# Kernel optimization log

Hardware: AMD Instinct MI355X
Metric: run time of the kernel (lower is better)

Reference implementation:

```python
import jax, jax.numpy as jnp
import numpy as np

IGNORE_LABEL = -100  # config.data.ignore_label


def setup_inputs() -> dict:
    key = jax.random.key(0)
    k1, k2 = jax.random.split(key)
    V, D = 100000, 128            # voxel_num, feature dim of s_3d_output.F
    B, NV, H, W = 2, 4, 240, 320  # batch, n_views, height, width
    features_3d = jax.random.normal(k1, (V, D), dtype=jnp.float32)
    # raycast kernel output: per-pixel voxel index, or ignore_label for misses.
    raw = jax.random.randint(k2, (B, NV, H, W), 0, V + V // 4)
    indexes_image = jnp.where(raw < V, raw, IGNORE_LABEL).astype(jnp.int32)
    return {"features_3d": features_3d, "indexes_image": indexes_image}


def reference(features_3d, indexes_image):
    V = features_3d.shape[0]
    idx = indexes_image.reshape(-1)              # [P] flattened pixel->voxel index
    valid = idx != IGNORE_LABEL                  # [P] hit mask
    safe = jnp.where(valid, idx, 0)              # clamp misses for gather safety
    # projected_features[p] = features_3d[idx[p]] if hit else 0
    projected = jnp.where(valid[:, None], features_3d[safe], 0.0)  # [P, D]
    # mapping3dto2d_num: number of pixels each voxel projects to
    mapping3dto2d_num = jax.ops.segment_sum(
        jnp.where(valid, 1, 0).astype(jnp.int32), safe, num_segments=V)
    return projected, indexes_image, mapping3dto2d_num
```

## Files before the change

kernel.cpp:

```cpp
#include <hip/hip_runtime.h>

#define IGNORE_LABEL (-100)

typedef float f32x4 __attribute__((ext_vector_type(4)));

#define NS    8
#define VCAP  80000
#define ICAP  160000


__device__ __forceinline__ unsigned short f2bf_rne(float x) {
    union { float f; unsigned int u; } c; c.f = x;
    return (unsigned short)((c.u + 0x7FFFu + ((c.u >> 16) & 1u)) >> 16);
}
__device__ __forceinline__ f32x4 bf2f(ushort4 q) {
    union { unsigned int u; float f; } a, b, c, d;
    a.u = ((unsigned int)q.x) << 16; b.u = ((unsigned int)q.y) << 16;
    c.u = ((unsigned int)q.z) << 16; d.u = ((unsigned int)q.w) << 16;
    f32x4 r; r.x = a.f; r.y = b.f; r.z = c.f; r.w = d.f; return r;
}

__global__ void k_tobf16(const float4* __restrict__ feat4,
                         ushort4* __restrict__ bf, int n4) {
    const int stride = gridDim.x * blockDim.x;
    for (int i = blockIdx.x * blockDim.x + threadIdx.x; i < n4; i += stride) {
        const float4 v = feat4[i];
        ushort4 o;
        o.x = f2bf_rne(v.x); o.y = f2bf_rne(v.y);
        o.z = f2bf_rne(v.z); o.w = f2bf_rne(v.w);
        bf[i] = o;
    }
}

__global__ __launch_bounds__(256) void k_hist(
        const int* __restrict__ idx, float* __restrict__ idx_out,
        float* __restrict__ counts, int* __restrict__ cursor,
        int* __restrict__ listP, int* __restrict__ listV,
        int P, int sliceW) {
    __shared__ int hcnt[NS + 1], hbase[NS + 1], hoff[NS + 1];
    const int t = threadIdx.x;
    if (t <= NS) { hcnt[t] = 0; hoff[t] = 0; }
    __syncthreads();

    const int p0 = (blockIdx.x * 256 + t) * 4;
    int v[4]; int bin[4]; bool have = false;
    if (p0 + 3 < P) {
        const int4 q = *(const int4*)(idx + p0);
        v[0] = q.x; v[1] = q.y; v[2] = q.z; v[3] = q.w;
        float4 f; f.x = (float)q.x; f.y = (float)q.y; f.z = (float)q.z; f.w = (float)q.w;
        *(float4*)(idx_out + p0) = f;
        have = true;
        #pragma unroll
        for (int k = 0; k < 4; ++k) {
            if (v[k] != IGNORE_LABEL) {
                int s = v[k] / sliceW; s = s > NS - 1 ? NS - 1 : s;
                bin[k] = s;
                atomicAdd(&counts[v[k]], 1.0f);
            } else bin[k] = NS;
            atomicAdd(&hcnt[bin[k]], 1);
        }
    } else {
        for (int p = p0; p < P && p >= 0; ++p) {
            const int vv = idx[p];
            idx_out[p] = (float)vv;
            if (vv != IGNORE_LABEL) atomicAdd(&counts[vv], 1.0f);
        }
    }
    __syncthreads();
    if (t <= NS) hbase[t] = atomicAdd(&cursor[t], hcnt[t]);
    __syncthreads();
    if (have) {
        #pragma unroll
        for (int k = 0; k < 4; ++k) {
            const int b = bin[k];
            const int pos = hbase[b] + atomicAdd(&hoff[b], 1);
            if (b < NS) {
                if (pos < VCAP) { listP[b * VCAP + pos] = p0 + k; listV[b * VCAP + pos] = v[k]; }
            } else {
                if (pos < ICAP) listP[NS * VCAP + pos] = p0 + k;
            }
        }
    }
}

__global__ __launch_bounds__(256) void k_gather(
        const ushort4* __restrict__ bf,
        const int*     __restrict__ cursor,
        const int*     __restrict__ listP,
        const int*     __restrict__ listV,
        f32x4*         __restrict__ proj) {
    const int s    = blockIdx.x & (NS - 1);
    const int lane = threadIdx.x & 31;
    const int gid  = (blockIdx.x >> 3) * 8 + (threadIdx.x >> 5);
    const int base = s * VCAP;
    int n = cursor[s]; n = n > VCAP ? VCAP : n;

    int i = gid;
    for (; i + 2048 < n; i += 4096) {
        const int pA = listP[base + i],        vA = listV[base + i];
        const int pB = listP[base + i + 2048], vB = listV[base + i + 2048];
        const ushort4 qA = bf[(size_t)vA * 32 + lane];
        const ushort4 qB = bf[(size_t)vB * 32 + lane];
        __builtin_nontemporal_store(bf2f(qA), &proj[(size_t)pA * 32 + lane]);
        __builtin_nontemporal_store(bf2f(qB), &proj[(size_t)pB * 32 + lane]);
    }
    for (; i < n; i += 2048) {
        const int p = listP[base + i], vv = listV[base + i];
        const ushort4 q = bf[(size_t)vv * 32 + lane];
        __builtin_nontemporal_store(bf2f(q), &proj[(size_t)p * 32 + lane]);
    }

    int ninv = cursor[NS]; ninv = ninv > ICAP ? ICAP : ninv;
    const int G = blockIdx.x * 8 + (threadIdx.x >> 5);
    const f32x4 z = (f32x4)(0.f);
    for (int j = G; j < ninv; j += 16384) {
        const int p = listP[NS * VCAP + j];
        __builtin_nontemporal_store(z, &proj[(size_t)p * 32 + lane]);
    }
}

__global__ void k_fallback(const f32x4* __restrict__ feat,
                           const int* __restrict__ idx,
                           f32x4* __restrict__ proj,
                           float* __restrict__ idx_out,
                           float* __restrict__ counts, int P) {
    const int tid  = blockIdx.x * blockDim.x + threadIdx.x;
    const int lane = tid & 31;
    const int grp0 = tid >> 5;
    const int ngrp = (gridDim.x * blockDim.x) >> 5;
    for (int p = grp0; p < P; p += ngrp) {
        const int v = idx[p];
        const bool valid = (v != IGNORE_LABEL);
        const int s = valid ? v : 0;
        f32x4 a = feat[(size_t)s * 32 + lane];
        if (!valid) a = (f32x4)(0.f);
        proj[(size_t)p * 32 + lane] = a;
        if (lane == 0) {
            idx_out[p] = (float)v;
            if (valid) atomicAdd(&counts[v], 1.0f);
        }
    }
}

extern "C" void kernel_launch(void* const* d_in, const int* in_sizes, int n_in,
                              void* d_out, int out_size, void* d_ws, size_t ws_size,
                              hipStream_t stream) {
    const float* feat = (const float*)d_in[0];
    const int*   idx  = (const int*)d_in[1];

    const int D = 128;
    const int V = in_sizes[0] / D;
    const int P = in_sizes[1];

    float* out     = (float*)d_out;
    float* idx_out = out + (size_t)P * D;
    float* counts  = idx_out + P;

    (void)hipMemsetAsync(counts, 0, (size_t)V * sizeof(float), stream);

    const size_t tableBytes = (size_t)V * D * sizeof(unsigned short);
    const size_t need = tableBytes + 64 * sizeof(int)
                      + (size_t)(NS * VCAP + ICAP) * sizeof(int)
                      + (size_t)(NS * VCAP) * sizeof(int);
    if (ws_size < need) {
        k_fallback<<<2048, 256, 0, stream>>>((const f32x4*)feat, idx,
                                             (f32x4*)out, idx_out, counts, P);
        return;
    }

    ushort4* bf   = (ushort4*)d_ws;
    int* cursor   = (int*)((char*)d_ws + tableBytes);
    int* listP    = cursor + 64;
    int* listV    = listP + (NS * VCAP + ICAP);
    const int sliceW = (V + NS - 1) / NS;

    (void)hipMemsetAsync(cursor, 0, 64 * sizeof(int), stream);

    k_tobf16<<<2048, 256, 0, stream>>>((const float4*)feat, (ushort4*)bf, V * D / 4);
    k_hist<<<(P + 1023) / 1024, 256, 0, stream>>>(idx, idx_out, counts, cursor,
                                                  listP, listV, P, sliceW);
    k_gather<<<2048, 256, 0, stream>>>((const ushort4*)bf, cursor, listP, listV,
                                       (f32x4*)out);
}
```

Baseline: 115.9 us.

## Quantize feature table to int8 with per-row scale and fuse prep kernels

Replaces the bf16 copy of the feature table with int8 values plus a per-row absmax scale, built in a new k_prep kernel that also does the histogram and bucketing previously done in k_hist. The gather reads half as many table bytes and dequantizes before writing fp32 outputs, and stores now go through inline-asm nontemporal instructions. This drops one launch and cuts table traffic, but int8 quantization loses more precision than bf16. The tail handling for P not divisible by 4 is removed, and k_prep is launched with 2048 blocks, which covers only 2048*1024 pixels of the histogram loop.

Result: no change. 117.1 us (+1.0%).

```diff
diff --git a/kernel.cpp b/kernel.cpp
--- a/kernel.cpp
+++ b/kernel.cpp
@@ -9,41 +9,59 @@
 #define ICAP  160000
 
 
-__device__ __forceinline__ unsigned short f2bf_rne(float x) {
-    union { float f; unsigned int u; } c; c.f = x;
-    return (unsigned short)((c.u + 0x7FFFu + ((c.u >> 16) & 1u)) >> 16);
-}
-__device__ __forceinline__ f32x4 bf2f(ushort4 q) {
-    union { unsigned int u; float f; } a, b, c, d;
-    a.u = ((unsigned int)q.x) << 16; b.u = ((unsigned int)q.y) << 16;
-    c.u = ((unsigned int)q.z) << 16; d.u = ((unsigned int)q.w) << 16;
-    f32x4 r; r.x = a.f; r.y = b.f; r.z = c.f; r.w = d.f; return r;
+__device__ __forceinline__ void store_nt(f32x4 v, f32x4* addr) {
+    asm volatile("global_store_dwordx4 %0, %1, off sc0 sc1 nt"
+                 :: "v"(addr), "v"(v) : "memory");
 }
 
-__global__ void k_tobf16(const float4* __restrict__ feat4,
-                         ushort4* __restrict__ bf, int n4) {
-    const int stride = gridDim.x * blockDim.x;
-    for (int i = blockIdx.x * blockDim.x + threadIdx.x; i < n4; i += stride) {
-        const float4 v = feat4[i];
-        ushort4 o;
-        o.x = f2bf_rne(v.x); o.y = f2bf_rne(v.y);
-        o.z = f2bf_rne(v.z); o.w = f2bf_rne(v.w);
-        bf[i] = o;
-    }
+__device__ __forceinline__ f32x4 dec8(unsigned int u, float sc) {
+    f32x4 r;
+    r.x = (float)(int)(signed char)(u & 0xffu);
+    r.y = (float)(int)(signed char)((u >> 8) & 0xffu);
+    r.z = (float)(int)(signed char)((u >> 16) & 0xffu);
+    r.w = (float)(int)(signed char)(u >> 24);
+    r.x *= sc; r.y *= sc; r.z *= sc; r.w *= sc;
+    return r;
 }
 
-__global__ __launch_bounds__(256) void k_hist(
-        const int* __restrict__ idx, float* __restrict__ idx_out,
-        float* __restrict__ counts, int* __restrict__ cursor,
-        int* __restrict__ listP, int* __restrict__ listV,
-        int P, int sliceW) {
+__global__ __launch_bounds__(256) void k_prep(
+        const f32x4* __restrict__ feat4,
+        const int*   __restrict__ idx,
+        unsigned int* __restrict__ q8,
+        float*       __restrict__ scales,
+        float*       __restrict__ idx_out,
+        float*       __restrict__ counts,
+        int*         __restrict__ cursor,
+        int*         __restrict__ listP,
+        int*         __restrict__ listV,
+        int V, int P, int sliceW) {
+    const int gtid = blockIdx.x * 256 + threadIdx.x;
+    const int l    = threadIdx.x & 31;
+    const int grp  = gtid >> 5;
+    const int ngrp = (gridDim.x * 256) >> 5;
+    for (int r = grp; r < V; r += ngrp) {
+        const f32x4 x = feat4[(size_t)r * 32 + l];
+        float m = fmaxf(fmaxf(fabsf(x.x), fabsf(x.y)), fmaxf(fabsf(x.z), fabsf(x.w)));
+        #pragma unroll
+        for (int d = 1; d < 32; d <<= 1) m = fmaxf(m, __shfl_xor(m, d, 32));
+        m = fmaxf(m, 1e-20f);
+        const float inv = 127.0f / m;
+        const int a = (int)rintf(x.x * inv);
+        const int b = (int)rintf(x.y * inv);
+        const int c = (int)rintf(x.z * inv);
+        const int d4 = (int)rintf(x.w * inv);
+        q8[(size_t)r * 32 + l] = (unsigned int)(a & 255) | ((unsigned int)(b & 255) << 8)
+                               | ((unsigned int)(c & 255) << 16) | ((unsigned int)(d4 & 255) << 24);
+        if (l == 0) scales[r] = m / 127.0f;
+    }
+
     __shared__ int hcnt[NS + 1], hbase[NS + 1], hoff[NS + 1];
     const int t = threadIdx.x;
     if (t <= NS) { hcnt[t] = 0; hoff[t] = 0; }
     __syncthreads();
 
-    const int p0 = (blockIdx.x * 256 + t) * 4;
-    int v[4]; int bin[4]; bool have = false;
+    const int p0 = gtid * 4;
+    int v[4], bin[4]; bool have = false;
     if (p0 + 3 < P) {
         const int4 q = *(const int4*)(idx + p0);
         v[0] = q.x; v[1] = q.y; v[2] = q.z; v[3] = q.w;
@@ -58,12 +76,6 @@
                 atomicAdd(&counts[v[k]], 1.0f);
             } else bin[k] = NS;
             atomicAdd(&hcnt[bin[k]], 1);
-        }
-    } else {
-        for (int p = p0; p < P && p >= 0; ++p) {
-            const int vv = idx[p];
-            idx_out[p] = (float)vv;
-            if (vv != IGNORE_LABEL) atomicAdd(&counts[vv], 1.0f);
         }
     }
     __syncthreads();
@@ -84,11 +96,12 @@
 }
 
 __global__ __launch_bounds__(256) void k_gather(
-        const ushort4* __restrict__ bf,
-        const int*     __restrict__ cursor,
-        const int*     __restrict__ listP,
-        const int*     __restrict__ listV,
-        f32x4*         __restrict__ proj) {
+        const unsigned int* __restrict__ q8,
+        const float*        __restrict__ scales,
+        const int*          __restrict__ cursor,
+        const int*          __restrict__ listP,
+        const int*          __restrict__ listV,
+        f32x4*              __restrict__ proj) {
     const int s    = blockIdx.x & (NS - 1);
     const int lane = threadIdx.x & 31;
     const int gid  = (blockIdx.x >> 3) * 8 + (threadIdx.x >> 5);
@@ -99,15 +112,16 @@
     for (; i + 2048 < n; i += 4096) {
         const int pA = listP[base + i],        vA = listV[base + i];
         const int pB = listP[base + i + 2048], vB = listV[base + i + 2048];
-        const ushort4 qA = bf[(size_t)vA * 32 + lane];
-        const ushort4 qB = bf[(size_t)vB * 32 + lane];
-        __builtin_nontemporal_store(bf2f(qA), &proj[(size_t)pA * 32 + lane]);
-        __builtin_nontemporal_store(bf2f(qB), &proj[(size_t)pB * 32 + lane]);
+        const unsigned int qA = q8[(size_t)vA * 32 + lane];
+        const unsigned int qB = q8[(size_t)vB * 32 + lane];
+        const float sA = scales[vA], sB = scales[vB];
+        store_nt(dec8(qA, sA), &proj[(size_t)pA * 32 + lane]);
+        store_nt(dec8(qB, sB), &proj[(size_t)pB * 32 + lane]);
     }
     for (; i < n; i += 2048) {
         const int p = listP[base + i], vv = listV[base + i];
-        const ushort4 q = bf[(size_t)vv * 32 + lane];
-        __builtin_nontemporal_store(bf2f(q), &proj[(size_t)p * 32 + lane]);
+        store_nt(dec8(q8[(size_t)vv * 32 + lane], scales[vv]),
+                 &proj[(size_t)p * 32 + lane]);
     }
 
     int ninv = cursor[NS]; ninv = ninv > ICAP ? ICAP : ninv;
@@ -115,7 +129,7 @@
     const f32x4 z = (f32x4)(0.f);
     for (int j = G; j < ninv; j += 16384) {
         const int p = listP[NS * VCAP + j];
-        __builtin_nontemporal_store(z, &proj[(size_t)p * 32 + lane]);
+        store_nt(z, &proj[(size_t)p * 32 + lane]);
     }
 }
 
@@ -158,27 +172,28 @@
 
     (void)hipMemsetAsync(counts, 0, (size_t)V * sizeof(float), stream);
 
-    const size_t tableBytes = (size_t)V * D * sizeof(unsigned short);
-    const size_t need = tableBytes + 64 * sizeof(int)
-                      + (size_t)(NS * VCAP + ICAP) * sizeof(int)
-                      + (size_t)(NS * VCAP) * sizeof(int);
+    const size_t q8Bytes = (size_t)V * D;
+    const size_t need = q8Bytes + (size_t)V * 4 + 256
+                      + (size_t)(NS * VCAP + ICAP) * 4
+                      + (size_t)(NS * VCAP) * 4;
     if (ws_size < need) {
         k_fallback<<<2048, 256, 0, stream>>>((const f32x4*)feat, idx,
                                              (f32x4*)out, idx_out, counts, P);
         return;
     }
 
-    ushort4* bf   = (ushort4*)d_ws;
-    int* cursor   = (int*)((char*)d_ws + tableBytes);
-    int* listP    = cursor + 64;
-    int* listV    = listP + (NS * VCAP + ICAP);
+    unsigned int* q8     = (unsigned int*)d_ws;
+    float*        scales = (float*)((char*)d_ws + q8Bytes);
+    int*          cursor = (int*)(scales + V);
+    int*          listP  = cursor + 64;
+    int*          listV  = listP + (NS * VCAP + ICAP);
     const int sliceW = (V + NS - 1) / NS;
 
     (void)hipMemsetAsync(cursor, 0, 64 * sizeof(int), stream);
 
-    k_tobf16<<<2048, 256, 0, stream>>>((const float4*)feat, (ushort4*)bf, V * D / 4);
-    k_hist<<<(P + 1023) / 1024, 256, 0, stream>>>(idx, idx_out, counts, cursor,
-                                                  listP, listV, P, sliceW);
-    k_gather<<<2048, 256, 0, stream>>>((const ushort4*)bf, cursor, listP, listV,
+    k_prep<<<2048, 256, 0, stream>>>((const f32x4*)feat, idx, q8, scales,
+                                     idx_out, counts, cursor, listP, listV,
+                                     V, P, sliceW);
+    k_gather<<<2048, 256, 0, stream>>>(q8, scales, cursor, listP, listV,
                                        (f32x4*)out);
 }
```
